# Kernel optimization log

Hardware: AMD Instinct MI355X
Metric: run time of the kernel (lower is better)

## Reference

```python
import jax, jax.numpy as jnp
import numpy as np

B, T, I, H = 256, 2048, 1, 64


def setup_inputs() -> dict:
    key = jax.random.key(0)
    k_x, k_wi, k_wh, k_bi, k_bh = jax.random.split(key, 5)
    s = 1.0 / np.sqrt(H)  # PyTorch GRU init: U(-1/sqrt(H), 1/sqrt(H))
    return {
        "x": jax.random.normal(k_x, (B, T, I), dtype=jnp.float32),
        "W_ih": jax.random.uniform(k_wi, (3 * H, I), jnp.float32, -s, s),
        "W_hh": jax.random.uniform(k_wh, (3 * H, H), jnp.float32, -s, s),
        "b_ih": jax.random.uniform(k_bi, (3 * H,), jnp.float32, -s, s),
        "b_hh": jax.random.uniform(k_bh, (3 * H,), jnp.float32, -s, s),
    }


def reference(x, W_ih, W_hh, b_ih, b_hh):
    # x: [B, T, I]. PyTorch nn.GRU gate math (gate order: r, z, n).
    b, t, _ = x.shape
    h_dim = W_hh.shape[1]
    # Precompute all input-side gate projections: [B, T, 3H]
    xg = jnp.einsum('bti,gi->btg', x, W_ih) + b_ih
    xg_t = jnp.swapaxes(xg, 0, 1)  # [T, B, 3H] for scan

    def step(h, xg_step):
        gh = h @ W_hh.T + b_hh  # [B, 3H]
        xr, xz, xn = jnp.split(xg_step, 3, axis=-1)
        hr, hz, hn = jnp.split(gh, 3, axis=-1)
        r = jax.nn.sigmoid(xr + hr)
        z = jax.nn.sigmoid(xz + hz)
        n = jnp.tanh(xn + r * hn)
        h_new = (1.0 - z) * n + z * h
        # forward keeps only the LAST hidden channel per timestep (x[:, :, -1])
        return h_new, h_new[:, -1]

    h0 = jnp.zeros((b, h_dim), x.dtype)
    _, ys = jax.lax.scan(step, h0, xg_t)  # ys: [T, B]
    # final view(B, seq_len * feature_size) with feature_size=1 -> [B, T]
    return jnp.swapaxes(ys, 0, 1)
```

## Files before the change

### kernel.cpp

```cpp
#include <hip/hip_runtime.h>

#define B_ 256
#define T_ 2048
#define H_ 64

typedef float f32x4 __attribute__((ext_vector_type(4)));
typedef _Float16 h16x2 __attribute__((ext_vector_type(2)));

__device__ __forceinline__ float fdot2(h16x2 a, h16x2 b, float c) {
#if __has_builtin(__builtin_amdgcn_fdot2)
    return __builtin_amdgcn_fdot2(a, b, c, false);
#else
    float d;
    asm("v_dot2_f32_f16 %0, %1, %2, %3" : "=v"(d) : "v"(a), "v"(b), "v"(c));
    return d;
#endif
}

__device__ __forceinline__ float readlane_f(float v, int idx) {
    return __builtin_bit_cast(float,
        __builtin_amdgcn_readlane(__builtin_bit_cast(int, v), idx));
}

#define NLOG2E (-1.4426950408889634f)
#define TLOG2E ( 2.8853900817779268f)

__global__ __launch_bounds__(64, 1)
void gru_kernel(const float* __restrict__ x,
                const float* __restrict__ W_ih,
                const float* __restrict__ W_hh,
                const float* __restrict__ b_ih,
                const float* __restrict__ b_hh,
                float* __restrict__ out)
{
    __shared__ __align__(16) _Float16 shh[H_];

    const int lane = threadIdx.x;
    const int b    = blockIdx.x;

    h16x2 wr[32], wz[32], wn[32];
    {
        const f32x4* pr = (const f32x4*)(W_hh + (size_t)lane * H_);
        const f32x4* pz = (const f32x4*)(W_hh + (size_t)(64 + lane) * H_);
        const f32x4* pn = (const f32x4*)(W_hh + (size_t)(128 + lane) * H_);
        #pragma unroll
        for (int q = 0; q < 16; ++q) {
            f32x4 vr = pr[q], vz = pz[q], vn = pn[q];
            wr[2*q]   = h16x2{(_Float16)(NLOG2E * vr.x), (_Float16)(NLOG2E * vr.y)};
            wr[2*q+1] = h16x2{(_Float16)(NLOG2E * vr.z), (_Float16)(NLOG2E * vr.w)};
            wz[2*q]   = h16x2{(_Float16)(NLOG2E * vz.x), (_Float16)(NLOG2E * vz.y)};
            wz[2*q+1] = h16x2{(_Float16)(NLOG2E * vz.z), (_Float16)(NLOG2E * vz.w)};
            wn[2*q]   = h16x2{(_Float16)(TLOG2E * vn.x), (_Float16)(TLOG2E * vn.y)};
            wn[2*q+1] = h16x2{(_Float16)(TLOG2E * vn.z), (_Float16)(TLOG2E * vn.w)};
        }
    }
    #pragma unroll
    for (int i = 0; i < 32; ++i)
        asm volatile("" : "+v"(wr[i]), "+v"(wz[i]), "+v"(wn[i]));

    const float wihr = NLOG2E * W_ih[lane];
    const float wihz = NLOG2E * W_ih[64 + lane];
    const float wihn = TLOG2E * W_ih[128 + lane];
    const float br   = NLOG2E * (b_ih[lane]      + b_hh[lane]);
    const float bz   = NLOG2E * (b_ih[64 + lane] + b_hh[64 + lane]);
    const float bhn  = TLOG2E * b_hh[128 + lane];
    const float bin  = TLOG2E * b_ih[128 + lane];

    const float* __restrict__ xrow = x + (size_t)b * T_;
    float* __restrict__ orow = out + (size_t)b * T_;

    shh[lane] = (_Float16)0.0f;

    float h_own = 0.0f;
    float oval  = 0.0f;
    float xa = xrow[lane];
    float xb = 0.0f;

    for (int tb = 0; tb < T_ / 64; ++tb) {
        if (tb < T_ / 64 - 1) xb = xrow[(tb + 1) * 64 + lane];

        #pragma unroll 4
        for (int t2 = 0; t2 < 64; ++t2) {
            const float xt  = readlane_f(xa, t2);
            const float xpr = fmaf(xt, wihr, br);
            const float xpz = fmaf(xt, wihz, bz);
            const float xpn = fmaf(xt, wihn, bin);

            h16x2 hh[32];
            const f32x4* hp = (const f32x4*)shh;
            #pragma unroll
            for (int q = 0; q < 8; ++q) {
                union { f32x4 f; h16x2 h[4]; } u;
                u.f = hp[q];
                hh[4*q]   = u.h[0];
                hh[4*q+1] = u.h[1];
                hh[4*q+2] = u.h[2];
                hh[4*q+3] = u.h[3];
            }

            float ar[4] = {0,0,0,0};
            #pragma unroll
            for (int i = 0; i < 32; ++i) ar[i >> 3] = fdot2(wr[i], hh[i], ar[i >> 3]);
            float sr = ((ar[0] + ar[1]) + (ar[2] + ar[3])) + xpr;
            float r  = __builtin_amdgcn_rcpf(1.0f + __builtin_amdgcn_exp2f(sr));

            float az[4] = {0,0,0,0};
            #pragma unroll
            for (int i = 0; i < 32; ++i) az[i >> 3] = fdot2(wz[i], hh[i], az[i >> 3]);
            float sz = ((az[0] + az[1]) + (az[2] + az[3])) + xpz;
            float z  = __builtin_amdgcn_rcpf(1.0f + __builtin_amdgcn_exp2f(sz));

            float an[4] = {0,0,0,0};
            #pragma unroll
            for (int i = 0; i < 32; ++i) an[i >> 3] = fdot2(wn[i], hh[i], an[i >> 3]);
            float hn  = ((an[0] + an[1]) + (an[2] + an[3])) + bhn;
            float pre = fmaf(r, hn, xpn);
            float n   = fmaf(-2.0f, __builtin_amdgcn_rcpf(
                              1.0f + __builtin_amdgcn_exp2f(pre)), 1.0f);

            float h_new = fmaf(z, h_own - n, n);
            h_own = h_new;

            shh[lane] = (_Float16)h_new;

            float h63 = readlane_f(h_new, 63);
            oval = (t2 == lane) ? h63 : oval;
        }

        orow[tb * 64 + lane] = oval;
        xa = xb;
    }
}

extern "C" void kernel_launch(void* const* d_in, const int* in_sizes, int n_in,
                              void* d_out, int out_size, void* d_ws, size_t ws_size,
                              hipStream_t stream) {
    const float* x    = (const float*)d_in[0];
    const float* W_ih = (const float*)d_in[1];
    const float* W_hh = (const float*)d_in[2];
    const float* b_ih = (const float*)d_in[3];
    const float* b_hh = (const float*)d_in[4];
    float* out = (float*)d_out;

    dim3 grid(B_), block(64);
    gru_kernel<<<grid, block, 0, stream>>>(x, W_ih, W_hh, b_ih, b_hh, out);
}
```

Before: 619.9 us.

## Split recurrent matvec between MFMA and VALU dot2 paths

Splits each step's hidden-to-gate matvec across two compute units. Inputs 32..63 of the hidden state go through twelve 16x16x32 f16 MFMA instructions with weights held in registers, and inputs 0..31 stay on VALU fdot2. This halves the serial fdot2 chain, and the matrix core runs the other half alongside it. Because every row of the MFMA A operand is the same broadcast vector, most of the matrix work is redundant. The step still pays MFMA latency plus lane-select logic to pull the right output column.

Result: slower. 726.9 us (+17.3%).

```diff
diff --git a/kernel.cpp b/kernel.cpp
--- a/kernel.cpp
+++ b/kernel.cpp
@@ -6,6 +6,7 @@
 
 typedef float f32x4 __attribute__((ext_vector_type(4)));
 typedef _Float16 h16x2 __attribute__((ext_vector_type(2)));
+typedef _Float16 h16x8 __attribute__((ext_vector_type(8)));
 
 __device__ __forceinline__ float fdot2(h16x2 a, h16x2 b, float c) {
 #if __has_builtin(__builtin_amdgcn_fdot2)
@@ -36,15 +37,17 @@
     __shared__ __align__(16) _Float16 shh[H_];
 
     const int lane = threadIdx.x;
+    const int ln15 = lane & 15;
+    const int kg   = lane >> 4;
     const int b    = blockIdx.x;
 
-    h16x2 wr[32], wz[32], wn[32];
+    h16x2 wr[16], wz[16], wn[16];
     {
         const f32x4* pr = (const f32x4*)(W_hh + (size_t)lane * H_);
         const f32x4* pz = (const f32x4*)(W_hh + (size_t)(64 + lane) * H_);
         const f32x4* pn = (const f32x4*)(W_hh + (size_t)(128 + lane) * H_);
         #pragma unroll
-        for (int q = 0; q < 16; ++q) {
+        for (int q = 0; q < 8; ++q) {
             f32x4 vr = pr[q], vz = pz[q], vn = pn[q];
             wr[2*q]   = h16x2{(_Float16)(NLOG2E * vr.x), (_Float16)(NLOG2E * vr.y)};
             wr[2*q+1] = h16x2{(_Float16)(NLOG2E * vr.z), (_Float16)(NLOG2E * vr.w)};
@@ -55,8 +58,28 @@
         }
     }
     #pragma unroll
-    for (int i = 0; i < 32; ++i)
+    for (int i = 0; i < 16; ++i)
         asm volatile("" : "+v"(wr[i]), "+v"(wz[i]), "+v"(wn[i]));
+
+    h16x8 wbm[3][4];
+    #pragma unroll
+    for (int g = 0; g < 3; ++g) {
+        const float s = (g == 2) ? TLOG2E : NLOG2E;
+        #pragma unroll
+        for (int nt = 0; nt < 4; ++nt) {
+            const float* p = W_hh + (size_t)(g * 64 + nt * 16 + ln15) * H_
+                           + 32 + 8 * kg;
+            h16x8 v;
+            #pragma unroll
+            for (int j = 0; j < 8; ++j) v[j] = (_Float16)(s * p[j]);
+            wbm[g][nt] = v;
+        }
+    }
+    #pragma unroll
+    for (int g = 0; g < 3; ++g)
+        #pragma unroll
+        for (int nt = 0; nt < 4; ++nt)
+            asm volatile("" : "+v"(wbm[g][nt]));
 
     const float wihr = NLOG2E * W_ih[lane];
     const float wihz = NLOG2E * W_ih[64 + lane];
@@ -75,6 +98,9 @@
     float oval  = 0.0f;
     float xa = xrow[lane];
     float xb = 0.0f;
+    const f32x4 z4 = {0.f, 0.f, 0.f, 0.f};
+    const bool kb0 = (kg & 1) != 0;
+    const bool kb1 = (kg & 2) != 0;
 
     for (int tb = 0; tb < T_ / 64; ++tb) {
         if (tb < T_ / 64 - 1) xb = xrow[(tb + 1) * 64 + lane];
@@ -86,10 +112,11 @@
             const float xpz = fmaf(xt, wihz, bz);
             const float xpn = fmaf(xt, wihn, bin);
 
-            h16x2 hh[32];
+            h16x8 a1 = *(const h16x8*)&shh[32 + 8 * kg];
+            h16x2 hh[16];
             const f32x4* hp = (const f32x4*)shh;
             #pragma unroll
-            for (int q = 0; q < 8; ++q) {
+            for (int q = 0; q < 4; ++q) {
                 union { f32x4 f; h16x2 h[4]; } u;
                 u.f = hp[q];
                 hh[4*q]   = u.h[0];
@@ -98,22 +125,48 @@
                 hh[4*q+3] = u.h[3];
             }
 
-            float ar[4] = {0,0,0,0};
-            #pragma unroll
-            for (int i = 0; i < 32; ++i) ar[i >> 3] = fdot2(wr[i], hh[i], ar[i >> 3]);
-            float sr = ((ar[0] + ar[1]) + (ar[2] + ar[3])) + xpr;
-            float r  = __builtin_amdgcn_rcpf(1.0f + __builtin_amdgcn_exp2f(sr));
-
-            float az[4] = {0,0,0,0};
-            #pragma unroll
-            for (int i = 0; i < 32; ++i) az[i >> 3] = fdot2(wz[i], hh[i], az[i >> 3]);
-            float sz = ((az[0] + az[1]) + (az[2] + az[3])) + xpz;
-            float z  = __builtin_amdgcn_rcpf(1.0f + __builtin_amdgcn_exp2f(sz));
-
-            float an[4] = {0,0,0,0};
-            #pragma unroll
-            for (int i = 0; i < 32; ++i) an[i >> 3] = fdot2(wn[i], hh[i], an[i >> 3]);
-            float hn  = ((an[0] + an[1]) + (an[2] + an[3])) + bhn;
+            f32x4 mr[4], mz[4], mn[4];
+            #pragma unroll
+            for (int nt = 0; nt < 4; ++nt)
+                mr[nt] = __builtin_amdgcn_mfma_f32_16x16x32_f16(a1, wbm[0][nt], z4, 0, 0, 0);
+            #pragma unroll
+            for (int nt = 0; nt < 4; ++nt)
+                mz[nt] = __builtin_amdgcn_mfma_f32_16x16x32_f16(a1, wbm[1][nt], z4, 0, 0, 0);
+            #pragma unroll
+            for (int nt = 0; nt < 4; ++nt)
+                mn[nt] = __builtin_amdgcn_mfma_f32_16x16x32_f16(a1, wbm[2][nt], z4, 0, 0, 0);
+
+            float ar0 = 0.f, ar1 = 0.f;
+            #pragma unroll
+            for (int i = 0; i < 16; i += 2) {
+                ar0 = fdot2(wr[i],   hh[i],   ar0);
+                ar1 = fdot2(wr[i+1], hh[i+1], ar1);
+            }
+            float r01 = kb0 ? mr[1][0] : mr[0][0];
+            float r23 = kb0 ? mr[3][0] : mr[2][0];
+            float sr  = (ar0 + ar1) + (kb1 ? r23 : r01) + xpr;
+            float r   = __builtin_amdgcn_rcpf(1.0f + __builtin_amdgcn_exp2f(sr));
+
+            float az0 = 0.f, az1 = 0.f;
+            #pragma unroll
+            for (int i = 0; i < 16; i += 2) {
+                az0 = fdot2(wz[i],   hh[i],   az0);
+                az1 = fdot2(wz[i+1], hh[i+1], az1);
+            }
+            float z01 = kb0 ? mz[1][0] : mz[0][0];
+            float z23 = kb0 ? mz[3][0] : mz[2][0];
+            float sz  = (az0 + az1) + (kb1 ? z23 : z01) + xpz;
+            float z   = __builtin_amdgcn_rcpf(1.0f + __builtin_amdgcn_exp2f(sz));
+
+            float an0 = 0.f, an1 = 0.f;
+            #pragma unroll
+            for (int i = 0; i < 16; i += 2) {
+                an0 = fdot2(wn[i],   hh[i],   an0);
+                an1 = fdot2(wn[i+1], hh[i+1], an1);
+            }
+            float n01 = kb0 ? mn[1][0] : mn[0][0];
+            float n23 = kb0 ? mn[3][0] : mn[2][0];
+            float hn  = (an0 + an1) + (kb1 ? n23 : n01) + bhn;
             float pre = fmaf(r, hn, xpn);
             float n   = fmaf(-2.0f, __builtin_amdgcn_rcpf(
                               1.0f + __builtin_amdgcn_exp2f(pre)), 1.0f);
```
